# Kernel tuning notes

Hardware: AMD Instinct MI355X
Metric: run time of the kernel (lower is better)

The kernel has to match this reference:

```python
import jax, jax.numpy as jnp
import numpy as np
import math

B, C, D, H = 4, 1024, 1024, 16
DH = D // H  # dim_per_head = 64
TOPK_FRAC = 0.7
K = int(C * TOPK_FRAC)  # 716


def setup_inputs() -> dict:
    key = jax.random.key(0)
    ks = jax.random.split(key, 12)
    s = 1.0 / math.sqrt(D)
    return {
        "key": jax.random.normal(ks[0], (B, C, D), jnp.float32),
        "value": jax.random.normal(ks[1], (B, C, D), jnp.float32),
        "query": jax.random.normal(ks[2], (B, C, D), jnp.float32),
        "Wq": jax.random.normal(ks[3], (D, D), jnp.float32) * s,
        "bq": jax.random.normal(ks[4], (D,), jnp.float32) * s,
        "Wk": jax.random.normal(ks[5], (D, D), jnp.float32) * s,
        "bk": jax.random.normal(ks[6], (D,), jnp.float32) * s,
        "Wv": jax.random.normal(ks[7], (D, D), jnp.float32) * s,
        "bv": jax.random.normal(ks[8], (D,), jnp.float32) * s,
        "Wo": jax.random.normal(ks[9], (D, D), jnp.float32) * s,
        "bo": jax.random.normal(ks[10], (D,), jnp.float32) * s,
    }


def _split_heads(x):
    # [B, C, D] -> [B, H, C, DH]
    return x.reshape(B, C, H, DH).transpose(0, 2, 1, 3)


def reference(key, value, query, Wq, bq, Wk, bk, Wv, bv, Wo, bo):
    # QKV projections (torch Linear: x @ W.T + b)
    q = _split_heads(query @ Wq.T + bq) / math.sqrt(DH)
    k = _split_heads(key @ Wk.T + bk)
    v = _split_heads(value @ Wv.T + bv)

    # [B, H, C, C] attention scores
    scores = jnp.einsum('bhqd,bhkd->bhqk', q, k)

    # Top-k mask along last dim: keep entries >= k-th largest score per row.
    # (Equivalent to torch.topk + scatter for distinct float scores.)
    topk_vals = jax.lax.top_k(scores, K)[0]       # [B, H, C, K]
    thresh = topk_vals[..., -1:]                  # k-th largest
    scores1 = jnp.where(scores >= thresh, scores, -jnp.inf)

    attn = jax.nn.softmax(scores1, axis=-1)       # dropout is identity at eval
    ctx = jnp.einsum('bhqk,bhkd->bhqd', attn, v)  # [B, H, C, DH]
    ctx = ctx.transpose(0, 2, 1, 3).reshape(B, C, D)
    return ctx @ Wo.T + bo
```

## Files before the change

kernel.cpp:

```cpp
#include <hip/hip_runtime.h>
#include <hip/hip_bf16.h>
#include <stdint.h>

typedef __hip_bfloat16 bf16;
typedef short s16x8 __attribute__((ext_vector_type(8)));
typedef float f32x4 __attribute__((ext_vector_type(4)));

#define B_ 4
#define C_ 1024
#define D_ 1024
#define H_ 16
#define K_ 716

static __device__ __forceinline__ short f2b(float f) {
    __hip_bfloat16 h = __float2bfloat16(f);
    short s; __builtin_memcpy(&s, &h, 2); return s;
}
static __device__ __forceinline__ f32x4 mfma16(s16x8 a, s16x8 b, f32x4 c) {
    return __builtin_amdgcn_mfma_f32_16x16x32_bf16(a, b, c, 0, 0, 0);
}

__global__ __launch_bounds__(256, 3) void proj_gemm(
        const float* __restrict__ Aq, const float* __restrict__ Ak, const float* __restrict__ Av,
        const float* __restrict__ Wq, const float* __restrict__ Wk, const float* __restrict__ Wv,
        const float* __restrict__ bq, const float* __restrict__ bk, const float* __restrict__ bv,
        bf16* __restrict__ qb, bf16* __restrict__ kb, bf16* __restrict__ vT)
{
    __shared__ bf16 As[128 * 64];
    __shared__ bf16 Bs[128 * 64];
    const int z = blockIdx.z;
    const float* Ap = (z == 0) ? Aq : ((z == 1) ? Ak : Av);
    const float* Wp = (z == 0) ? Wq : ((z == 1) ? Wk : Wv);
    const float* bp = (z == 0) ? bq : ((z == 1) ? bk : bv);
    const int tid = threadIdx.x;
    const int l = tid & 63, w = tid >> 6, g = l >> 4, c = l & 15;
    const int wm = w & 1, wn = w >> 1;
    const int n0 = blockIdx.x * 128, m0 = blockIdx.y * 128;
    const int srow = tid >> 3, scol = (tid & 7) * 8;

    f32x4 acc[4][4] = {};

    for (int kt = 0; kt < 16; ++kt) {
        #pragma unroll
        for (int r = 0; r < 4; ++r) {
            const int row = r * 32 + srow;
            {
                const float* pa = Ap + (size_t)(m0 + row) * 1024 + kt * 64 + scol;
                float4 f0 = ((const float4*)pa)[0], f1 = ((const float4*)pa)[1];
                s16x8 v;
                v[0]=f2b(f0.x); v[1]=f2b(f0.y); v[2]=f2b(f0.z); v[3]=f2b(f0.w);
                v[4]=f2b(f1.x); v[5]=f2b(f1.y); v[6]=f2b(f1.z); v[7]=f2b(f1.w);
                *(s16x8*)&As[row * 64 + scol] = v;
            }
            {
                const float* pb = Wp + (size_t)(n0 + row) * 1024 + kt * 64 + scol;
                float4 f0 = ((const float4*)pb)[0], f1 = ((const float4*)pb)[1];
                s16x8 v;
                v[0]=f2b(f0.x); v[1]=f2b(f0.y); v[2]=f2b(f0.z); v[3]=f2b(f0.w);
                v[4]=f2b(f1.x); v[5]=f2b(f1.y); v[6]=f2b(f1.z); v[7]=f2b(f1.w);
                *(s16x8*)&Bs[row * 64 + scol] = v;
            }
        }
        __syncthreads();
        #pragma unroll
        for (int kk = 0; kk < 2; ++kk) {
            s16x8 af[4], bfv[4];
            #pragma unroll
            for (int i = 0; i < 4; ++i)
                af[i] = *(const s16x8*)&As[(wm * 64 + i * 16 + c) * 64 + kk * 32 + g * 8];
            #pragma unroll
            for (int j = 0; j < 4; ++j)
                bfv[j] = *(const s16x8*)&Bs[(wn * 64 + j * 16 + c) * 64 + kk * 32 + g * 8];
            #pragma unroll
            for (int i = 0; i < 4; ++i)
                #pragma unroll
                for (int j = 0; j < 4; ++j)
                    acc[i][j] = mfma16(af[i], bfv[j], acc[i][j]);
        }
        __syncthreads();
    }
    const float scale = (z == 0) ? 0.125f : 1.0f;
    #pragma unroll
    for (int j = 0; j < 4; ++j) {
        const int coln = n0 + wn * 64 + j * 16 + c;
        const float bias = bp[coln];
        #pragma unroll
        for (int i = 0; i < 4; ++i) {
            #pragma unroll
            for (int jj = 0; jj < 4; ++jj) {
                const int rowm = m0 + wm * 64 + i * 16 + g * 4 + jj;
                const float val = (acc[i][j][jj] + bias) * scale;
                if (z == 0) {
                    qb[(size_t)rowm * 1024 + coln] = __float2bfloat16(val);
                } else if (z == 1) {
                    kb[(size_t)rowm * 1024 + coln] = __float2bfloat16(val);
                } else {
                    const int b = rowm >> 10, n = rowm & 1023;
                    const int h = coln >> 6, dh = coln & 63;
                    vT[((size_t)((b * H_ + h) * 64 + dh) << 10) + n] = __float2bfloat16(val);
                }
            }
        }
    }
}

__global__ __launch_bounds__(256, 4) void out_gemm(
        const bf16* __restrict__ Ab, const float* __restrict__ W,
        const float* __restrict__ bias, float* __restrict__ out)
{
    __shared__ bf16 As[64 * 64];
    __shared__ bf16 Bs[128 * 64];
    const int tid = threadIdx.x;
    const int l = tid & 63, w = tid >> 6, g = l >> 4, c = l & 15;
    const int n0 = blockIdx.x * 128, m0 = blockIdx.y * 64;
    const int srow = tid >> 3, scol = (tid & 7) * 8;

    f32x4 acc[4][2] = {};

    for (int kt = 0; kt < 16; ++kt) {
        #pragma unroll
        for (int r = 0; r < 2; ++r) {
            const int row = r * 32 + srow;
            *(s16x8*)&As[row * 64 + scol] =
                *(const s16x8*)(Ab + (size_t)(m0 + row) * 1024 + kt * 64 + scol);
        }
        #pragma unroll
        for (int r = 0; r < 4; ++r) {
            const int row = r * 32 + srow;
            const float* pb = W + (size_t)(n0 + row) * 1024 + kt * 64 + scol;
            float4 f0 = ((const float4*)pb)[0], f1 = ((const float4*)pb)[1];
            s16x8 v;
            v[0]=f2b(f0.x); v[1]=f2b(f0.y); v[2]=f2b(f0.z); v[3]=f2b(f0.w);
            v[4]=f2b(f1.x); v[5]=f2b(f1.y); v[6]=f2b(f1.z); v[7]=f2b(f1.w);
            *(s16x8*)&Bs[row * 64 + scol] = v;
        }
        __syncthreads();
        #pragma unroll
        for (int kk = 0; kk < 2; ++kk) {
            s16x8 af[4], bfv[2];
            #pragma unroll
            for (int i = 0; i < 4; ++i)
                af[i] = *(const s16x8*)&As[(i * 16 + c) * 64 + kk * 32 + g * 8];
            #pragma unroll
            for (int j = 0; j < 2; ++j)
                bfv[j] = *(const s16x8*)&Bs[(w * 32 + j * 16 + c) * 64 + kk * 32 + g * 8];
            #pragma unroll
            for (int i = 0; i < 4; ++i)
                #pragma unroll
                for (int j = 0; j < 2; ++j)
                    acc[i][j] = mfma16(af[i], bfv[j], acc[i][j]);
        }
        __syncthreads();
    }
    #pragma unroll
    for (int j = 0; j < 2; ++j) {
        const int coln = n0 + w * 32 + j * 16 + c;
        const float bv = bias[coln];
        #pragma unroll
        for (int i = 0; i < 4; ++i)
            #pragma unroll
            for (int jj = 0; jj < 4; ++jj) {
                const int rowm = m0 + i * 16 + g * 4 + jj;
                out[(size_t)rowm * 1024 + coln] = acc[i][j][jj] + bv;
            }
    }
}

#define LOADROW(UM, MXOUT, RR)                                                  \
    int UM[16]; int MXOUT;                                                      \
    {                                                                           \
        const int szr = ((RR) & 7) << 4;                                        \
        uint4 xa = *(const uint4*)((const char*)S + (RR) * 2048 + ((l * 16) ^ szr));          \
        uint4 xb = *(const uint4*)((const char*)S + (RR) * 2048 + ((1024 + l * 16) ^ szr));   \
        unsigned xs[8] = {xa.x, xa.y, xa.z, xa.w, xb.x, xb.y, xb.z, xb.w};      \
        _Pragma("unroll")                                                       \
        for (int q = 0; q < 8; ++q) {                                           \
            unsigned x = xs[q];                                                 \
            unsigned mmk = 0x80008000u | (((x >> 15) & 0x00010001u) * 0x7FFFu); \
            unsigned y = x ^ mmk;                                               \
            UM[2 * q]     = (int)(y & 0xFFFFu);                                 \
            UM[2 * q + 1] = (int)(y >> 16);                                     \
        }                                                                       \
        int mx = 0;                                                             \
        _Pragma("unroll")                                                       \
        for (int q = 0; q < 16; ++q) mx = max(mx, UM[q]);                       \
        _Pragma("unroll")                                                       \
        for (int off = 32; off; off >>= 1) mx = max(mx, __shfl_xor(mx, off));   \
        MXOUT = mx;                                                             \
    }

#define PROCROW(UM, MX, PP, RR)                                                 \
    {                                                                           \
        const int rawm = ((MX) & 0x8000) ? ((MX) ^ 0x8000) : ((~(MX)) & 0xFFFF);\
        const float smax = __uint_as_float(((unsigned)rawm) << 16);             \
        float e[16]; float ls = 0.f;                                            \
        _Pragma("unroll")                                                       \
        for (int j = 0; j < 16; ++j) {                                          \
            const int v = UM[j];                                                \
            const int rb = (v & 0x8000) ? (v ^ 0x8000) : ((~v) & 0xFFFF);       \
            const float s = __uint_as_float(((unsigned)rb) << 16);              \
            const float ee = __expf(s - smax);                                  \
            e[j] = (v >= (PP)) ? ee : 0.f;                                      \
            ls += e[j];                                                         \
        }                                                                       \
        _Pragma("unroll")                                                       \
        for (int off = 32; off; off >>= 1) ls += __shfl_xor(ls, off);           \
        const float inv = 1.0f / ls;                                            \
        unsigned o[8];                                                          \
        _Pragma("unroll")                                                       \
        for (int jp = 0; jp < 8; ++jp) {                                        \
            const unsigned lo = (unsigned short)f2b(e[2 * jp] * inv);           \
            const unsigned hi = (unsigned short)f2b(e[2 * jp + 1] * inv);       \
            o[jp] = lo | (hi << 16);                                            \
        }                                                                       \
        const int szr = ((RR) & 7) << 4;                                        \
        *(uint4*)((char*)S + (RR) * 2048 + ((l * 16) ^ szr)) = make_uint4(o[0], o[1], o[2], o[3]); \
        *(uint4*)((char*)S + (RR) * 2048 + ((1024 + l * 16) ^ szr)) = make_uint4(o[4], o[5], o[6], o[7]); \
    }

__global__ __launch_bounds__(512, 4) void attn_topk(
        const bf16* __restrict__ qb, const bf16* __restrict__ kb,
        const bf16* __restrict__ vT, bf16* __restrict__ ctx)
{
    __shared__ bf16 S[32 * 1024];
    const int bid = blockIdx.x;
    const int wid = (bid & 7) * 256 + (bid >> 3);
    const int qt = wid & 31, h = (wid >> 5) & 15, b = wid >> 9;
    const int qr0 = qt * 32;
    const int tid = threadIdx.x, w = tid >> 6, l = tid & 63, g = l >> 4, c = l & 15;

    const size_t batchoff = (size_t)b * C_ * D_;
    const bf16* qrow  = qb + batchoff + (size_t)qr0 * 1024 + h * 64;
    const bf16* kbase = kb + batchoff + h * 64;

    s16x8 aq[2][2];
    #pragma unroll
    for (int m = 0; m < 2; ++m)
        #pragma unroll
        for (int kk = 0; kk < 2; ++kk)
            aq[m][kk] = *(const s16x8*)(qrow + (size_t)(m * 16 + c) * 1024 + kk * 32 + g * 8);

    auto ldk = [&](int nf, int kk) {
        const int ncol = w * 128 + nf * 16;
        return *(const s16x8*)(kbase + (size_t)(ncol + c) * 1024 + kk * 32 + g * 8);
    };
    s16x8 b0 = ldk(0, 0), b1 = ldk(0, 1);
    #pragma unroll 1
    for (int nf = 0; nf < 8; ++nf) {
        s16x8 nb0 = b0, nb1 = b1;
        if (nf < 7) { nb0 = ldk(nf + 1, 0); nb1 = ldk(nf + 1, 1); }
        const int ncol = w * 128 + nf * 16;
        #pragma unroll
        for (int m = 0; m < 2; ++m) {
            f32x4 accS = {0.f, 0.f, 0.f, 0.f};
            accS = mfma16(aq[m][0], b0, accS);
            accS = mfma16(aq[m][1], b1, accS);
            #pragma unroll
            for (int jj = 0; jj < 4; ++jj) {
                const int row = m * 16 + g * 4 + jj;
                *(bf16*)((char*)S + row * 2048 + (((ncol + c) * 2) ^ ((row & 7) << 4))) =
                    __float2bfloat16(accS[jj]);
            }
        }
        b0 = nb0; b1 = nb1;
    }
    __syncthreads();

    #pragma unroll 1
    for (int pr = 0; pr < 2; ++pr) {
        const int r0 = w * 4 + pr * 2, r1 = r0 + 1;
        LOADROW(um0, mx0, r0)
        LOADROW(um1, mx1, r1)
        int p0 = 0, p1 = 0;
        #pragma unroll 1
        for (int bit = 15; bit >= 0; --bit) {
            const int t0 = p0 | (1 << bit), t1 = p1 | (1 << bit);
            int c0 = 0, c1 = 0;
            #pragma unroll
            for (int j = 0; j < 16; ++j) {
                c0 += __popcll(__ballot(um0[j] >= t0));
                c1 += __popcll(__ballot(um1[j] >= t1));
            }
            if (c0 >= K_) p0 = t0;
            if (c1 >= K_) p1 = t1;
        }
        PROCROW(um0, mx0, p0, r0)
        PROCROW(um1, mx1, p1, r1)
    }
    __syncthreads();

    {
        const int m = w & 1, nt = w >> 1;
        const bf16* vb = vT + ((size_t)((b * H_ + h) * 64 + nt * 16 + c) << 10) + g * 8;
        const int srow = m * 16 + c;
        const int ssz = (srow & 7) << 4;
        s16x8 c0 = *(const s16x8*)(vb + 0 * 32);
        s16x8 c1 = *(const s16x8*)(vb + 1 * 32);
        s16x8 c2 = *(const s16x8*)(vb + 2 * 32);
        s16x8 c3 = *(const s16x8*)(vb + 3 * 32);
        f32x4 acc = {0.f, 0.f, 0.f, 0.f};
        #pragma unroll 1
        for (int kt4 = 0; kt4 < 8; ++kt4) {
            s16x8 n0 = c0, n1 = c1, n2 = c2, n3 = c3;
            if (kt4 < 7) {
                n0 = *(const s16x8*)(vb + (kt4 * 4 + 4) * 32);
                n1 = *(const s16x8*)(vb + (kt4 * 4 + 5) * 32);
                n2 = *(const s16x8*)(vb + (kt4 * 4 + 6) * 32);
                n3 = *(const s16x8*)(vb + (kt4 * 4 + 7) * 32);
            }
            #pragma unroll
            for (int u = 0; u < 4; ++u) {
                const s16x8 af = *(const s16x8*)((const char*)S + srow * 2048 +
                                    ((((kt4 * 4 + u) * 64) + g * 16) ^ ssz));
                const s16x8 bv = (u == 0) ? c0 : (u == 1) ? c1 : (u == 2) ? c2 : c3;
                acc = mfma16(af, bv, acc);
            }
            c0 = n0; c1 = n1; c2 = n2; c3 = n3;
        }
        #pragma unroll
        for (int jj = 0; jj < 4; ++jj) {
            const int row = m * 16 + g * 4 + jj;
            ctx[batchoff + (size_t)(qr0 + row) * 1024 + h * 64 + nt * 16 + c] =
                __float2bfloat16(acc[jj]);
        }
    }
}

extern "C" void kernel_launch(void* const* d_in, const int* in_sizes, int n_in,
                              void* d_out, int out_size, void* d_ws, size_t ws_size,
                              hipStream_t stream)
{
    const float* key   = (const float*)d_in[0];
    const float* value = (const float*)d_in[1];
    const float* query = (const float*)d_in[2];
    const float* Wq = (const float*)d_in[3];
    const float* bq = (const float*)d_in[4];
    const float* Wk = (const float*)d_in[5];
    const float* bk = (const float*)d_in[6];
    const float* Wv = (const float*)d_in[7];
    const float* bv = (const float*)d_in[8];
    const float* Wo = (const float*)d_in[9];
    const float* bo = (const float*)d_in[10];

    char* ws = (char*)d_ws;
    bf16* qb   = (bf16*)(ws);
    bf16* kb   = (bf16*)(ws + (8u  << 20));
    bf16* vT   = (bf16*)(ws + (16u << 20));
    bf16* ctxb = (bf16*)(ws + (24u << 20));

    hipLaunchKernelGGL(proj_gemm, dim3(8, 32, 3), dim3(256), 0, stream,
                       query, key, value, Wq, Wk, Wv, bq, bk, bv, qb, kb, vT);
    hipLaunchKernelGGL(attn_topk, dim3(2048), dim3(512), 0, stream, qb, kb, vT, ctxb);
    hipLaunchKernelGGL(out_gemm, dim3(8, 64), dim3(256), 0, stream, ctxb, Wo, bo, (float*)d_out);
}
```

Before: 369.7 us.

## Pre-convert inputs to bf16, stage GEMM tiles via direct global-to-LDS loads, shrink attention tiles

Adds a conversion kernel that turns the activations and all four weight matrices into bf16 up front. The projection and output GEMMs then load swizzled tiles with global_load_lds instead of doing fp32 loads and conversions inside the main loop. The output GEMM tile shape changes to 128x64. The attention kernel moves from 32-row, 512-thread blocks to 16-row, 256-thread blocks, and each wave runs the radix threshold search on four rows at once. This removes per-tile conversion work from the GEMMs and raises attention occupancy, at the price of an extra full read/write pass over 64 MB of fp32 inputs.

```diff
diff --git a/kernel.cpp b/kernel.cpp
--- a/kernel.cpp
+++ b/kernel.cpp
@@ -19,58 +19,83 @@
 static __device__ __forceinline__ f32x4 mfma16(s16x8 a, s16x8 b, f32x4 c) {
     return __builtin_amdgcn_mfma_f32_16x16x32_bf16(a, b, c, 0, 0, 0);
 }
-
-__global__ __launch_bounds__(256, 3) void proj_gemm(
-        const float* __restrict__ Aq, const float* __restrict__ Ak, const float* __restrict__ Av,
-        const float* __restrict__ Wq, const float* __restrict__ Wk, const float* __restrict__ Wv,
+static __device__ __forceinline__ void gl_lds16(const void* g, void* l) {
+    __builtin_amdgcn_global_load_lds((const __attribute__((address_space(1))) void*)g,
+                                     (__attribute__((address_space(3))) void*)l, 16, 0, 0);
+}
+
+__global__ __launch_bounds__(256) void cvt_pass(
+        const float* __restrict__ q, const float* __restrict__ k, const float* __restrict__ v,
+        const float* __restrict__ wq, const float* __restrict__ wk,
+        const float* __restrict__ wv, const float* __restrict__ wo,
+        bf16* __restrict__ xq, bf16* __restrict__ xk, bf16* __restrict__ xv,
+        bf16* __restrict__ owq, bf16* __restrict__ owk, bf16* __restrict__ owv,
+        bf16* __restrict__ owo)
+{
+    const int nchunk = 16777216 / 8;
+    for (int cid = blockIdx.x * 256 + threadIdx.x; cid < nchunk; cid += gridDim.x * 256) {
+        const int e = cid * 8;
+        const float* src; bf16* dst; int off;
+        if      (e < 4194304)  { src = q;  dst = xq;  off = e; }
+        else if (e < 8388608)  { src = k;  dst = xk;  off = e - 4194304; }
+        else if (e < 12582912) { src = v;  dst = xv;  off = e - 8388608; }
+        else if (e < 13631488) { src = wq; dst = owq; off = e - 12582912; }
+        else if (e < 14680064) { src = wk; dst = owk; off = e - 13631488; }
+        else if (e < 15728640) { src = wv; dst = owv; off = e - 14680064; }
+        else                   { src = wo; dst = owo; off = e - 15728640; }
+        float4 f0 = ((const float4*)(src + off))[0];
+        float4 f1 = ((const float4*)(src + off))[1];
+        s16x8 o;
+        o[0]=f2b(f0.x); o[1]=f2b(f0.y); o[2]=f2b(f0.z); o[3]=f2b(f0.w);
+        o[4]=f2b(f1.x); o[5]=f2b(f1.y); o[6]=f2b(f1.z); o[7]=f2b(f1.w);
+        *(s16x8*)(dst + off) = o;
+    }
+}
+
+template<int ROWS>
+static __device__ __forceinline__ void stage_tile(const bf16* gtile, bf16* lds, int tid) {
+    #pragma unroll
+    for (int u = 0; u < ROWS / 32; ++u) {
+        const int lin  = u * 4096 + tid * 16;
+        const int row  = lin >> 7;
+        const int colb = (lin & 127) ^ ((row & 7) << 4);
+        gl_lds16((const char*)(gtile + (size_t)row * 1024) + colb,
+                 (char*)lds + (lin & ~1023));
+    }
+}
+#define LDS_FRAG(buf, row, kk) \
+    (*(const s16x8*)((const char*)(buf) + (row) * 128 + (((kk) * 64 + g * 16) ^ (((row) & 7) << 4))))
+
+__global__ __launch_bounds__(256, 4) void proj_gemm(
+        const bf16* __restrict__ xq, const bf16* __restrict__ xk, const bf16* __restrict__ xv,
+        const bf16* __restrict__ wqb, const bf16* __restrict__ wkb, const bf16* __restrict__ wvb,
         const float* __restrict__ bq, const float* __restrict__ bk, const float* __restrict__ bv,
         bf16* __restrict__ qb, bf16* __restrict__ kb, bf16* __restrict__ vT)
 {
     __shared__ bf16 As[128 * 64];
     __shared__ bf16 Bs[128 * 64];
     const int z = blockIdx.z;
-    const float* Ap = (z == 0) ? Aq : ((z == 1) ? Ak : Av);
-    const float* Wp = (z == 0) ? Wq : ((z == 1) ? Wk : Wv);
+    const bf16* Ap = (z == 0) ? xq : ((z == 1) ? xk : xv);
+    const bf16* Wp = (z == 0) ? wqb : ((z == 1) ? wkb : wvb);
     const float* bp = (z == 0) ? bq : ((z == 1) ? bk : bv);
     const int tid = threadIdx.x;
     const int l = tid & 63, w = tid >> 6, g = l >> 4, c = l & 15;
     const int wm = w & 1, wn = w >> 1;
     const int n0 = blockIdx.x * 128, m0 = blockIdx.y * 128;
-    const int srow = tid >> 3, scol = (tid & 7) * 8;
 
     f32x4 acc[4][4] = {};
 
     for (int kt = 0; kt < 16; ++kt) {
-        #pragma unroll
-        for (int r = 0; r < 4; ++r) {
-            const int row = r * 32 + srow;
-            {
-                const float* pa = Ap + (size_t)(m0 + row) * 1024 + kt * 64 + scol;
-                float4 f0 = ((const float4*)pa)[0], f1 = ((const float4*)pa)[1];
-                s16x8 v;
-                v[0]=f2b(f0.x); v[1]=f2b(f0.y); v[2]=f2b(f0.z); v[3]=f2b(f0.w);
-                v[4]=f2b(f1.x); v[5]=f2b(f1.y); v[6]=f2b(f1.z); v[7]=f2b(f1.w);
-                *(s16x8*)&As[row * 64 + scol] = v;
-            }
-            {
-                const float* pb = Wp + (size_t)(n0 + row) * 1024 + kt * 64 + scol;
-                float4 f0 = ((const float4*)pb)[0], f1 = ((const float4*)pb)[1];
-                s16x8 v;
-                v[0]=f2b(f0.x); v[1]=f2b(f0.y); v[2]=f2b(f0.z); v[3]=f2b(f0.w);
-                v[4]=f2b(f1.x); v[5]=f2b(f1.y); v[6]=f2b(f1.z); v[7]=f2b(f1.w);
-                *(s16x8*)&Bs[row * 64 + scol] = v;
-            }
-        }
+        stage_tile<128>(Ap + (size_t)m0 * 1024 + kt * 64, As, tid);
+        stage_tile<128>(Wp + (size_t)n0 * 1024 + kt * 64, Bs, tid);
         __syncthreads();
         #pragma unroll
         for (int kk = 0; kk < 2; ++kk) {
             s16x8 af[4], bfv[4];
             #pragma unroll
-            for (int i = 0; i < 4; ++i)
-                af[i] = *(const s16x8*)&As[(wm * 64 + i * 16 + c) * 64 + kk * 32 + g * 8];
-            #pragma unroll
-            for (int j = 0; j < 4; ++j)
-                bfv[j] = *(const s16x8*)&Bs[(wn * 64 + j * 16 + c) * 64 + kk * 32 + g * 8];
+            for (int i = 0; i < 4; ++i) af[i]  = LDS_FRAG(As, wm * 64 + i * 16 + c, kk);
+            #pragma unroll
+            for (int j = 0; j < 4; ++j) bfv[j] = LDS_FRAG(Bs, wn * 64 + j * 16 + c, kk);
             #pragma unroll
             for (int i = 0; i < 4; ++i)
                 #pragma unroll
@@ -105,45 +130,29 @@
 }
 
 __global__ __launch_bounds__(256, 4) void out_gemm(
-        const bf16* __restrict__ Ab, const float* __restrict__ W,
+        const bf16* __restrict__ Ab, const bf16* __restrict__ Wb,
         const float* __restrict__ bias, float* __restrict__ out)
 {
-    __shared__ bf16 As[64 * 64];
-    __shared__ bf16 Bs[128 * 64];
+    __shared__ bf16 As[128 * 64];
+    __shared__ bf16 Bs[64 * 64];
     const int tid = threadIdx.x;
     const int l = tid & 63, w = tid >> 6, g = l >> 4, c = l & 15;
-    const int n0 = blockIdx.x * 128, m0 = blockIdx.y * 64;
-    const int srow = tid >> 3, scol = (tid & 7) * 8;
+    const int wm = w & 1, wn = w >> 1;
+    const int n0 = blockIdx.x * 64, m0 = blockIdx.y * 128;
 
     f32x4 acc[4][2] = {};
 
     for (int kt = 0; kt < 16; ++kt) {
-        #pragma unroll
-        for (int r = 0; r < 2; ++r) {
-            const int row = r * 32 + srow;
-            *(s16x8*)&As[row * 64 + scol] =
-                *(const s16x8*)(Ab + (size_t)(m0 + row) * 1024 + kt * 64 + scol);
-        }
-        #pragma unroll
-        for (int r = 0; r < 4; ++r) {
-            const int row = r * 32 + srow;
-            const float* pb = W + (size_t)(n0 + row) * 1024 + kt * 64 + scol;
-            float4 f0 = ((const float4*)pb)[0], f1 = ((const float4*)pb)[1];
-            s16x8 v;
-            v[0]=f2b(f0.x); v[1]=f2b(f0.y); v[2]=f2b(f0.z); v[3]=f2b(f0.w);
-            v[4]=f2b(f1.x); v[5]=f2b(f1.y); v[6]=f2b(f1.z); v[7]=f2b(f1.w);
-            *(s16x8*)&Bs[row * 64 + scol] = v;
-        }
+        stage_tile<128>(Ab + (size_t)m0 * 1024 + kt * 64, As, tid);
+        stage_tile<64>(Wb + (size_t)n0 * 1024 + kt * 64, Bs, tid);
         __syncthreads();
         #pragma unroll
         for (int kk = 0; kk < 2; ++kk) {
             s16x8 af[4], bfv[2];
             #pragma unroll
-            for (int i = 0; i < 4; ++i)
-                af[i] = *(const s16x8*)&As[(i * 16 + c) * 64 + kk * 32 + g * 8];
-            #pragma unroll
-            for (int j = 0; j < 2; ++j)
-                bfv[j] = *(const s16x8*)&Bs[(w * 32 + j * 16 + c) * 64 + kk * 32 + g * 8];
+            for (int i = 0; i < 4; ++i) af[i]  = LDS_FRAG(As, wm * 64 + i * 16 + c, kk);
+            #pragma unroll
+            for (int j = 0; j < 2; ++j) bfv[j] = LDS_FRAG(Bs, wn * 32 + j * 16 + c, kk);
             #pragma unroll
             for (int i = 0; i < 4; ++i)
                 #pragma unroll
@@ -154,154 +163,147 @@
     }
     #pragma unroll
     for (int j = 0; j < 2; ++j) {
-        const int coln = n0 + w * 32 + j * 16 + c;
+        const int coln = n0 + wn * 32 + j * 16 + c;
         const float bv = bias[coln];
         #pragma unroll
         for (int i = 0; i < 4; ++i)
             #pragma unroll
             for (int jj = 0; jj < 4; ++jj) {
-                const int rowm = m0 + i * 16 + g * 4 + jj;
+                const int rowm = m0 + wm * 64 + i * 16 + g * 4 + jj;
                 out[(size_t)rowm * 1024 + coln] = acc[i][j][jj] + bv;
             }
     }
 }
 
-#define LOADROW(UM, MXOUT, RR)                                                  \
-    int UM[16]; int MXOUT;                                                      \
-    {                                                                           \
-        const int szr = ((RR) & 7) << 4;                                        \
-        uint4 xa = *(const uint4*)((const char*)S + (RR) * 2048 + ((l * 16) ^ szr));          \
-        uint4 xb = *(const uint4*)((const char*)S + (RR) * 2048 + ((1024 + l * 16) ^ szr));   \
-        unsigned xs[8] = {xa.x, xa.y, xa.z, xa.w, xb.x, xb.y, xb.z, xb.w};      \
-        _Pragma("unroll")                                                       \
-        for (int q = 0; q < 8; ++q) {                                           \
-            unsigned x = xs[q];                                                 \
-            unsigned mmk = 0x80008000u | (((x >> 15) & 0x00010001u) * 0x7FFFu); \
-            unsigned y = x ^ mmk;                                               \
-            UM[2 * q]     = (int)(y & 0xFFFFu);                                 \
-            UM[2 * q + 1] = (int)(y >> 16);                                     \
-        }                                                                       \
-        int mx = 0;                                                             \
-        _Pragma("unroll")                                                       \
-        for (int q = 0; q < 16; ++q) mx = max(mx, UM[q]);                       \
-        _Pragma("unroll")                                                       \
-        for (int off = 32; off; off >>= 1) mx = max(mx, __shfl_xor(mx, off));   \
-        MXOUT = mx;                                                             \
-    }
-
-#define PROCROW(UM, MX, PP, RR)                                                 \
-    {                                                                           \
-        const int rawm = ((MX) & 0x8000) ? ((MX) ^ 0x8000) : ((~(MX)) & 0xFFFF);\
-        const float smax = __uint_as_float(((unsigned)rawm) << 16);             \
-        float e[16]; float ls = 0.f;                                            \
-        _Pragma("unroll")                                                       \
-        for (int j = 0; j < 16; ++j) {                                          \
-            const int v = UM[j];                                                \
-            const int rb = (v & 0x8000) ? (v ^ 0x8000) : ((~v) & 0xFFFF);       \
-            const float s = __uint_as_float(((unsigned)rb) << 16);              \
-            const float ee = __expf(s - smax);                                  \
-            e[j] = (v >= (PP)) ? ee : 0.f;                                      \
-            ls += e[j];                                                         \
-        }                                                                       \
-        _Pragma("unroll")                                                       \
-        for (int off = 32; off; off >>= 1) ls += __shfl_xor(ls, off);           \
-        const float inv = 1.0f / ls;                                            \
-        unsigned o[8];                                                          \
-        _Pragma("unroll")                                                       \
-        for (int jp = 0; jp < 8; ++jp) {                                        \
-            const unsigned lo = (unsigned short)f2b(e[2 * jp] * inv);           \
-            const unsigned hi = (unsigned short)f2b(e[2 * jp + 1] * inv);       \
-            o[jp] = lo | (hi << 16);                                            \
-        }                                                                       \
-        const int szr = ((RR) & 7) << 4;                                        \
-        *(uint4*)((char*)S + (RR) * 2048 + ((l * 16) ^ szr)) = make_uint4(o[0], o[1], o[2], o[3]); \
-        *(uint4*)((char*)S + (RR) * 2048 + ((1024 + l * 16) ^ szr)) = make_uint4(o[4], o[5], o[6], o[7]); \
-    }
-
-__global__ __launch_bounds__(512, 4) void attn_topk(
+__global__ __launch_bounds__(256, 5) void attn_topk(
         const bf16* __restrict__ qb, const bf16* __restrict__ kb,
         const bf16* __restrict__ vT, bf16* __restrict__ ctx)
 {
-    __shared__ bf16 S[32 * 1024];
+    __shared__ bf16 S[16 * 1024];
     const int bid = blockIdx.x;
-    const int wid = (bid & 7) * 256 + (bid >> 3);
-    const int qt = wid & 31, h = (wid >> 5) & 15, b = wid >> 9;
-    const int qr0 = qt * 32;
+    const int wid = (bid & 7) * 512 + (bid >> 3);
+    const int qt = wid & 63, h = (wid >> 6) & 15, b = wid >> 10;
+    const int qr0 = qt * 16;
     const int tid = threadIdx.x, w = tid >> 6, l = tid & 63, g = l >> 4, c = l & 15;
 
     const size_t batchoff = (size_t)b * C_ * D_;
     const bf16* qrow  = qb + batchoff + (size_t)qr0 * 1024 + h * 64;
     const bf16* kbase = kb + batchoff + h * 64;
 
-    s16x8 aq[2][2];
-    #pragma unroll
-    for (int m = 0; m < 2; ++m)
-        #pragma unroll
-        for (int kk = 0; kk < 2; ++kk)
-            aq[m][kk] = *(const s16x8*)(qrow + (size_t)(m * 16 + c) * 1024 + kk * 32 + g * 8);
+    s16x8 aq[2];
+    #pragma unroll
+    for (int kk = 0; kk < 2; ++kk)
+        aq[kk] = *(const s16x8*)(qrow + (size_t)c * 1024 + kk * 32 + g * 8);
 
     auto ldk = [&](int nf, int kk) {
-        const int ncol = w * 128 + nf * 16;
+        const int ncol = w * 256 + nf * 16;
         return *(const s16x8*)(kbase + (size_t)(ncol + c) * 1024 + kk * 32 + g * 8);
     };
     s16x8 b0 = ldk(0, 0), b1 = ldk(0, 1);
     #pragma unroll 1
-    for (int nf = 0; nf < 8; ++nf) {
+    for (int nf = 0; nf < 16; ++nf) {
         s16x8 nb0 = b0, nb1 = b1;
-        if (nf < 7) { nb0 = ldk(nf + 1, 0); nb1 = ldk(nf + 1, 1); }
-        const int ncol = w * 128 + nf * 16;
-        #pragma unroll
-        for (int m = 0; m < 2; ++m) {
-            f32x4 accS = {0.f, 0.f, 0.f, 0.f};
-            accS = mfma16(aq[m][0], b0, accS);
-            accS = mfma16(aq[m][1], b1, accS);
-            #pragma unroll
-            for (int jj = 0; jj < 4; ++jj) {
-                const int row = m * 16 + g * 4 + jj;
-                *(bf16*)((char*)S + row * 2048 + (((ncol + c) * 2) ^ ((row & 7) << 4))) =
-                    __float2bfloat16(accS[jj]);
-            }
+        if (nf < 15) { nb0 = ldk(nf + 1, 0); nb1 = ldk(nf + 1, 1); }
+        const int ncol = w * 256 + nf * 16;
+        f32x4 accS = {0.f, 0.f, 0.f, 0.f};
+        accS = mfma16(aq[0], b0, accS);
+        accS = mfma16(aq[1], b1, accS);
+        #pragma unroll
+        for (int jj = 0; jj < 4; ++jj) {
+            const int row = g * 4 + jj;
+            *(bf16*)((char*)S + row * 2048 + (((ncol + c) * 2) ^ (row << 4))) =
+                __float2bfloat16(accS[jj]);
         }
         b0 = nb0; b1 = nb1;
     }
     __syncthreads();
 
+    int um[4][16]; int mx[4];
+    #pragma unroll
+    for (int i = 0; i < 4; ++i) {
+        const int r = w * 4 + i;
+        const int swz = r << 4;
+        uint4 xa = *(const uint4*)((const char*)S + r * 2048 + ((l * 16) ^ swz));
+        uint4 xb = *(const uint4*)((const char*)S + r * 2048 + ((1024 + l * 16) ^ swz));
+        unsigned xs[8] = {xa.x, xa.y, xa.z, xa.w, xb.x, xb.y, xb.z, xb.w};
+        int m = 0;
+        #pragma unroll
+        for (int q = 0; q < 8; ++q) {
+            unsigned x = xs[q];
+            unsigned mmk = 0x80008000u | (((x >> 15) & 0x00010001u) * 0x7FFFu);
+            unsigned y = x ^ mmk;
+            um[i][2 * q]     = (int)(y & 0xFFFFu);
+            um[i][2 * q + 1] = (int)(y >> 16);
+            m = max(m, max(um[i][2 * q], um[i][2 * q + 1]));
+        }
+        #pragma unroll
+        for (int off = 32; off; off >>= 1) m = max(m, __shfl_xor(m, off));
+        mx[i] = m;
+    }
+    int p0 = 0, p1 = 0, p2 = 0, p3 = 0;
     #pragma unroll 1
-    for (int pr = 0; pr < 2; ++pr) {
-        const int r0 = w * 4 + pr * 2, r1 = r0 + 1;
-        LOADROW(um0, mx0, r0)
-        LOADROW(um1, mx1, r1)
-        int p0 = 0, p1 = 0;
-        #pragma unroll 1
-        for (int bit = 15; bit >= 0; --bit) {
-            const int t0 = p0 | (1 << bit), t1 = p1 | (1 << bit);
-            int c0 = 0, c1 = 0;
-            #pragma unroll
-            for (int j = 0; j < 16; ++j) {
-                c0 += __popcll(__ballot(um0[j] >= t0));
-                c1 += __popcll(__ballot(um1[j] >= t1));
-            }
-            if (c0 >= K_) p0 = t0;
-            if (c1 >= K_) p1 = t1;
-        }
-        PROCROW(um0, mx0, p0, r0)
-        PROCROW(um1, mx1, p1, r1)
+    for (int bit = 15; bit >= 0; --bit) {
+        const int t0 = p0 | (1 << bit), t1 = p1 | (1 << bit);
+        const int t2 = p2 | (1 << bit), t3 = p3 | (1 << bit);
+        int c0 = 0, c1 = 0, c2 = 0, c3 = 0;
+        #pragma unroll
+        for (int j = 0; j < 16; ++j) {
+            c0 += __popcll(__ballot(um[0][j] >= t0));
+            c1 += __popcll(__ballot(um[1][j] >= t1));
+            c2 += __popcll(__ballot(um[2][j] >= t2));
+            c3 += __popcll(__ballot(um[3][j] >= t3));
+        }
+        if (c0 >= K_) p0 = t0;
+        if (c1 >= K_) p1 = t1;
+        if (c2 >= K_) p2 = t2;
+        if (c3 >= K_) p3 = t3;
+    }
+    const int pp[4] = {p0, p1, p2, p3};
+    #pragma unroll
+    for (int i = 0; i < 4; ++i) {
+        const int r = w * 4 + i;
+        const int MX = mx[i], PP = pp[i];
+        const int rawm = (MX & 0x8000) ? (MX ^ 0x8000) : ((~MX) & 0xFFFF);
+        const float smax = __uint_as_float(((unsigned)rawm) << 16);
+        float e[16]; float ls = 0.f;
+        #pragma unroll
+        for (int j = 0; j < 16; ++j) {
+            const int v = um[i][j];
+            const int rb = (v & 0x8000) ? (v ^ 0x8000) : ((~v) & 0xFFFF);
+            const float s = __uint_as_float(((unsigned)rb) << 16);
+            const float ee = __expf(s - smax);
+            e[j] = (v >= PP) ? ee : 0.f;
+            ls += e[j];
+        }
+        #pragma unroll
+        for (int off = 32; off; off >>= 1) ls += __shfl_xor(ls, off);
+        const float inv = 1.0f / ls;
+        unsigned o[8];
+        #pragma unroll
+        for (int jp = 0; jp < 8; ++jp) {
+            const unsigned lo = (unsigned short)f2b(e[2 * jp] * inv);
+            const unsigned hi = (unsigned short)f2b(e[2 * jp + 1] * inv);
+            o[jp] = lo | (hi << 16);
+        }
+        const int swz = r << 4;
+        *(uint4*)((char*)S + r * 2048 + ((l * 16) ^ swz)) = make_uint4(o[0], o[1], o[2], o[3]);
+        *(uint4*)((char*)S + r * 2048 + ((1024 + l * 16) ^ swz)) = make_uint4(o[4], o[5], o[6], o[7]);
     }
     __syncthreads();
 
     {
-        const int m = w & 1, nt = w >> 1;
+        const int nt = w;
         const bf16* vb = vT + ((size_t)((b * H_ + h) * 64 + nt * 16 + c) << 10) + g * 8;
-        const int srow = m * 16 + c;
-        const int ssz = (srow & 7) << 4;
-        s16x8 c0 = *(const s16x8*)(vb + 0 * 32);
-        s16x8 c1 = *(const s16x8*)(vb + 1 * 32);
-        s16x8 c2 = *(const s16x8*)(vb + 2 * 32);
-        s16x8 c3 = *(const s16x8*)(vb + 3 * 32);
+        const int srow = c;
+        const int ssz = srow << 4;
+        s16x8 v0 = *(const s16x8*)(vb + 0 * 32);
+        s16x8 v1 = *(const s16x8*)(vb + 1 * 32);
+        s16x8 v2 = *(const s16x8*)(vb + 2 * 32);
+        s16x8 v3 = *(const s16x8*)(vb + 3 * 32);
         f32x4 acc = {0.f, 0.f, 0.f, 0.f};
         #pragma unroll 1
         for (int kt4 = 0; kt4 < 8; ++kt4) {
-            s16x8 n0 = c0, n1 = c1, n2 = c2, n3 = c3;
+            s16x8 n0 = v0, n1 = v1, n2 = v2, n3 = v3;
             if (kt4 < 7) {
                 n0 = *(const s16x8*)(vb + (kt4 * 4 + 4) * 32);
                 n1 = *(const s16x8*)(vb + (kt4 * 4 + 5) * 32);
@@ -312,14 +314,14 @@
             for (int u = 0; u < 4; ++u) {
                 const s16x8 af = *(const s16x8*)((const char*)S + srow * 2048 +
                                     ((((kt4 * 4 + u) * 64) + g * 16) ^ ssz));
-                const s16x8 bv = (u == 0) ? c0 : (u == 1) ? c1 : (u == 2) ? c2 : c3;
+                const s16x8 bv = (u == 0) ? v0 : (u == 1) ? v1 : (u == 2) ? v2 : v3;
                 acc = mfma16(af, bv, acc);
             }
-            c0 = n0; c1 = n1; c2 = n2; c3 = n3;
+            v0 = n0; v1 = n1; v2 = n2; v3 = n3;
         }
         #pragma unroll
         for (int jj = 0; jj < 4; ++jj) {
-            const int row = m * 16 + g * 4 + jj;
+            const int row = g * 4 + jj;
             ctx[batchoff + (size_t)(qr0 + row) * 1024 + h * 64 + nt * 16 + c] =
                 __float2bfloat16(acc[jj]);
         }
@@ -346,10 +348,20 @@
     bf16* qb   = (bf16*)(ws);
     bf16* kb   = (bf16*)(ws + (8u  << 20));
     bf16* vT   = (bf16*)(ws + (16u << 20));
-    bf16* ctxb = (bf16*)(ws + (24u << 20));
-
+    bf16* xq   = (bf16*)(ws + (24u << 20));
+    bf16* xk   = (bf16*)(ws + (32u << 20));
+    bf16* xv   = (bf16*)(ws + (40u << 20));
+    bf16* wqb  = (bf16*)(ws + (48u << 20));
+    bf16* wkb  = (bf16*)(ws + (50u << 20));
+    bf16* wvb  = (bf16*)(ws + (52u << 20));
+    bf16* wob  = (bf16*)(ws + (54u << 20));
+    bf16* ctxb = xq;
+
+    hipLaunchKernelGGL(cvt_pass, dim3(2048), dim3(256), 0, stream,
+                       query, key, value, Wq, Wk, Wv, Wo,
+                       xq, xk, xv, wqb, wkb, wvb, wob);
     hipLaunchKernelGGL(proj_gemm, dim3(8, 32, 3), dim3(256), 0, stream,
-                       query, key, value, Wq, Wk, Wv, bq, bk, bv, qb, kb, vT);
-    hipLaunchKernelGGL(attn_topk, dim3(2048), dim3(512), 0, stream, qb, kb, vT, ctxb);
-    hipLaunchKernelGGL(out_gemm, dim3(8, 64), dim3(256), 0, stream, ctxb, Wo, bo, (float*)d_out);
-}
+                       xq, xk, xv, wqb, wkb, wvb, bq, bk, bv, qb, kb, vT);
+    hipLaunchKernelGGL(attn_topk, dim3(4096), dim3(256), 0, stream, qb, kb, vT, ctxb);
+    hipLaunchKernelGGL(out_gemm, dim3(16, 32), dim3(256), 0, stream, ctxb, wob, bo, (float*)d_out);
+}
```

After: 386.5 us. 4.5% more time.
